# Optimization experiments

Hardware: AMD Instinct MI355X
Metric: run time of the kernel (lower is better)

Reference implementation:

```python
import jax, jax.numpy as jnp
import numpy as np

N = 100000      # nodes
E = 6400000     # edges (avg degree 64)
S = 8           # FSM states
X = 2 ** S      # neighborhood 'characters' (256)
ITERS = 20      # NeuralFSM.iterations


def setup_inputs() -> dict:
    key = jax.random.key(0)
    k1, k2, k3 = jax.random.split(key, 3)
    # one-hot initial node states [N, S]
    state_idx = jax.random.randint(k1, (N,), 0, S)
    s0 = jax.nn.one_hot(state_idx, S, dtype=jnp.float32)
    # edge list [2, E]
    edge_index = jax.random.randint(k2, (2, E), 0, N, dtype=jnp.int32)
    # FSM transition tensor T[char, state, :] is one-hot over next state -> [X, S, S]
    next_state = jax.random.randint(k3, (X, S), 0, S)
    T = jax.nn.one_hot(next_state, S, dtype=jnp.float32)
    return {"s0": s0, "edge_index": edge_index, "T": T}


def reference(s0, edge_index, T):
    n_nodes, n_states = s0.shape
    src, dst = edge_index[0], edge_index[1]
    powers = (2 ** jnp.arange(n_states)).astype(jnp.int32)  # base-2 encoding of thresholded aggr

    def step(s, _):
        # message = x_j gathered from source nodes, scatter-added at destinations
        msg_sum = jax.ops.segment_sum(s[src], dst, num_segments=n_nodes)  # [N, S]
        # threshold (> 0.5) then clamp to {0,1}
        aggr = (msg_sum > 0.5).astype(jnp.int32)                          # [N, S]
        # multiple-hot -> index into 2^S characters (one-hot folded into a gather)
        idx = aggr @ powers                                               # [N]
        # einsum('x,s,xst->t') with one-hot char == gather T[idx] then contract state
        new_s = jnp.einsum('ns,nst->nt', s, T[idx])                       # [N, S]
        return new_s, None

    s_final, _ = jax.lax.scan(step, s0, None, length=ITERS)
    return s_final
```

## Files before the change

### kernel.cpp

```cpp
#include <hip/hip_runtime.h>
#include <hip/hip_bf16.h>
#include <stdint.h>


#define NN 100000
#define EE 6400000
#define NCHARS 2048
#define ITERS 20

#define NBKT 250
#define NPB 400
#define WPS 12500
#define X4N 3125
#define CEDGE 12800
#define NCHUNK 500
#define PCAP 13312

#define BLINES 25
#define BAR_ARR(i) ((i) * 16)
#define BAR_TOP    800
#define BAR_REL(i) (832 + (i) * 16)
#define BAR_WORDS  2048

typedef uint32_t u32x4 __attribute__((ext_vector_type(4)));

__global__ void decode_kernel(const float* __restrict__ s0,
                              const float* __restrict__ T,
                              uint32_t* __restrict__ gPk0,
                              uint8_t* __restrict__ nextT,
                              uint32_t* __restrict__ bar) {
    int i = blockIdx.x * blockDim.x + threadIdx.x;
    int stride = gridDim.x * blockDim.x;
    for (int j = i; j < BAR_WORDS; j += stride) bar[j] = 0u;
    if (i < NCHARS) {
        const float* row = T + i * 8;
        int t = 0;
        #pragma unroll
        for (int k = 1; k < 8; ++k) if (row[k] > 0.5f) t = k;
        nextT[i] = (uint8_t)t;
    }
    for (int j = i; j < WPS; j += stride) {
        uint32_t wv = 0;
        const float* rows = s0 + (size_t)j * 64;
        #pragma unroll
        for (int k = 0; k < 8; ++k) {
            const float* row = rows + k * 8;
            int s = 0;
            #pragma unroll
            for (int q = 1; q < 8; ++q) if (row[q] > 0.5f) s = q;
            wv |= (uint32_t)s << (k << 2);
        }
        gPk0[j] = wv;
    }
}

__global__ void __launch_bounds__(512) p1_hist(const int* __restrict__ dst,
                                               uint32_t* __restrict__ hist) {
    __shared__ uint32_t cw[8][256];
    int t = threadIdx.x, w = t >> 6;
    int c = blockIdx.x;
    for (int i = t; i < 8 * 256; i += 512) ((uint32_t*)cw)[i] = 0;
    __syncthreads();
    const int4* p = (const int4*)(dst + c * CEDGE);
    for (int i = t; i < CEDGE / 4; i += 512) {
        int4 d = p[i];
        atomicAdd(&cw[w][d.x / NPB], 1u);
        atomicAdd(&cw[w][d.y / NPB], 1u);
        atomicAdd(&cw[w][d.z / NPB], 1u);
        atomicAdd(&cw[w][d.w / NPB], 1u);
    }
    __syncthreads();
    for (int b = t; b < NBKT; b += 512) {
        uint32_t s = 0;
        #pragma unroll
        for (int w2 = 0; w2 < 8; ++w2) s += cw[w2][b];
        hist[(size_t)c * NBKT + b] = s;
    }
}

__global__ void p2a_scan(uint32_t* __restrict__ hist, uint32_t* __restrict__ total) {
    __shared__ uint32_t lds[256];
    int t = threadIdx.x;
    int b = blockIdx.x;
    uint32_t carry = 0;
    for (int c0 = 0; c0 < NCHUNK; c0 += 256) {
        int c = c0 + t;
        uint32_t v = (c < NCHUNK) ? hist[(size_t)c * NBKT + b] : 0u;
        lds[t] = v;
        __syncthreads();
        for (int off = 1; off < 256; off <<= 1) {
            uint32_t x = (t >= off) ? lds[t - off] : 0u;
            __syncthreads();
            lds[t] += x;
            __syncthreads();
        }
        if (c < NCHUNK) hist[(size_t)c * NBKT + b] = lds[t] - v + carry;
        uint32_t tot = lds[255];
        __syncthreads();
        carry += tot;
    }
    if (t == 0) total[b] = carry;
}

__global__ void p2b_scan(const uint32_t* __restrict__ total,
                         uint32_t* __restrict__ bucket_base) {
    __shared__ uint32_t lds[512];
    int t = threadIdx.x;
    uint32_t v = (t < NBKT) ? total[t] : 0u;
    lds[t] = v;
    __syncthreads();
    for (int off = 1; off < 512; off <<= 1) {
        uint32_t x = (t >= off) ? lds[t - off] : 0u;
        __syncthreads();
        lds[t] += x;
        __syncthreads();
    }
    if (t < NBKT) bucket_base[t] = lds[t] - v;
    if (t == 511) bucket_base[NBKT] = lds[511];
}

__global__ void __launch_bounds__(512) p3_partition(const int* __restrict__ src,
                                                    const int* __restrict__ dst,
                                                    const uint32_t* __restrict__ hist,
                                                    const uint32_t* __restrict__ bucket_base,
                                                    uint32_t* __restrict__ csr) {
    __shared__ uint32_t stage[CEDGE];
    __shared__ uint32_t cw[8][256];
    __shared__ uint32_t loc[NBKT + 1];
    __shared__ uint32_t segoff[NBKT];
    __shared__ uint32_t scanb[512];
    int t = threadIdx.x, w = t >> 6;
    int c = blockIdx.x;
    int e0 = c * CEDGE;
    const int4* ps4 = (const int4*)(src + e0);
    const int4* pd4 = (const int4*)(dst + e0);
    for (int i = t; i < 8 * 256; i += 512) ((uint32_t*)cw)[i] = 0;
    __syncthreads();
    for (int i = t; i < CEDGE / 4; i += 512) {
        int4 d = pd4[i];
        atomicAdd(&cw[w][d.x / NPB], 1u);
        atomicAdd(&cw[w][d.y / NPB], 1u);
        atomicAdd(&cw[w][d.z / NPB], 1u);
        atomicAdd(&cw[w][d.w / NPB], 1u);
    }
    __syncthreads();
    uint32_t tot = 0;
    if (t < NBKT) {
        #pragma unroll
        for (int w2 = 0; w2 < 8; ++w2) tot += cw[w2][t];
    }
    scanb[t] = tot;
    __syncthreads();
    for (int off = 1; off < 512; off <<= 1) {
        uint32_t x = (t >= off) ? scanb[t - off] : 0u;
        __syncthreads();
        scanb[t] += x;
        __syncthreads();
    }
    if (t < NBKT) {
        uint32_t excl = scanb[t] - tot;
        loc[t] = excl;
        segoff[t] = bucket_base[t] + hist[(size_t)c * NBKT + t] - excl;
        uint32_t acc = excl;
        #pragma unroll
        for (int w2 = 0; w2 < 8; ++w2) {
            uint32_t cv = cw[w2][t];
            cw[w2][t] = acc;
            acc += cv;
        }
    }
    if (t == 0) loc[NBKT] = CEDGE;
    __syncthreads();
    for (int i = t; i < CEDGE / 4; i += 512) {
        int4 d = pd4[i];
        int4 s = ps4[i];
        int bb; uint32_t dl, pos;
        bb = d.x / NPB; dl = (uint32_t)(d.x - bb * NPB);
        pos = atomicAdd(&cw[w][bb], 1u); stage[pos] = ((uint32_t)s.x << 9) | dl;
        bb = d.y / NPB; dl = (uint32_t)(d.y - bb * NPB);
        pos = atomicAdd(&cw[w][bb], 1u); stage[pos] = ((uint32_t)s.y << 9) | dl;
        bb = d.z / NPB; dl = (uint32_t)(d.z - bb * NPB);
        pos = atomicAdd(&cw[w][bb], 1u); stage[pos] = ((uint32_t)s.z << 9) | dl;
        bb = d.w / NPB; dl = (uint32_t)(d.w - bb * NPB);
        pos = atomicAdd(&cw[w][bb], 1u); stage[pos] = ((uint32_t)s.w << 9) | dl;
    }
    __syncthreads();
    for (int i = t; i < CEDGE; i += 512) {
        int lo = 0, hi = NBKT;
        while (hi - lo > 1) { int mid = (lo + hi) >> 1; if (loc[mid] <= (uint32_t)i) lo = mid; else hi = mid; }
        csr[segoff[lo] + (uint32_t)i] = stage[i];
    }
}

__global__ void __launch_bounds__(512) p4_sortsrc(uint32_t* __restrict__ csr,
                                                  const uint32_t* __restrict__ bucket_base) {
    __shared__ uint32_t st[PCAP];
    __shared__ uint32_t binh[512];
    int t = threadIdx.x;
    int j = blockIdx.x;
    int b = j >> 1, h = j & 1;
    uint32_t base = bucket_base[b], endb = bucket_base[b + 1];
    uint32_t n = endb - base;
    uint32_t n1 = (n + 1) >> 1;
    uint32_t r0 = h ? base + n1 : base;
    uint32_t cnt = h ? n - n1 : n1;
    if (cnt > PCAP) return;
    for (uint32_t i = t; i < cnt; i += 512) st[i] = csr[r0 + i];
    binh[t] = 0;
    __syncthreads();
    for (uint32_t i = t; i < cnt; i += 512) atomicAdd(&binh[st[i] >> 17], 1u);
    __syncthreads();
    uint32_t v = binh[t];
    __syncthreads();
    for (int off = 1; off < 512; off <<= 1) {
        uint32_t x = (t >= off) ? binh[t - off] : 0u;
        __syncthreads();
        binh[t] += x;
        __syncthreads();
    }
    uint32_t excl = binh[t] - v;
    __syncthreads();
    binh[t] = excl;
    __syncthreads();
    for (uint32_t i = t; i < cnt; i += 512) {
        uint32_t w = st[i];
        uint32_t pos = atomicAdd(&binh[w >> 17], 1u);
        csr[r0 + pos] = w;
    }
}

__global__ void __launch_bounds__(1024) mega_kernel(const uint32_t* __restrict__ csr,
                                                    const uint32_t* __restrict__ bucket_base,
                                                    uint32_t* __restrict__ gPkA,
                                                    uint32_t* __restrict__ gPkB,
                                                    const uint8_t* __restrict__ nextT,
                                                    float* __restrict__ out,
                                                    uint32_t* __restrict__ bar) {
    __shared__ uint32_t sPk[WPS];
    __shared__ uint32_t mask[NPB];
    __shared__ uint32_t packOwn[NPB / 8];
    __shared__ uint8_t  nT[NCHARS];
    __shared__ uint8_t  sown[NPB];
    int t = threadIdx.x;
    int b = blockIdx.x;
    uint32_t base = bucket_base[b];
    uint32_t end  = bucket_base[b + 1];

    if (t < 512) ((uint32_t*)nT)[t] = ((const uint32_t*)nextT)[t];
    const int line = b % BLINES;

    for (int p = 0; p < ITERS; ++p) {
        const uint32_t* curG = (p & 1) ? gPkB : gPkA;
        uint32_t*       nxtG = (p & 1) ? gPkA : gPkB;
        {
            const u32x4* g4 = (const u32x4*)curG;
            int i0 = t, i1 = t + 1024, i2 = t + 2048;
            int i3 = t + 3072; if (i3 > X4N - 1) i3 = X4N - 1;
            const u32x4 *p0 = g4 + i0, *p1 = g4 + i1, *p2 = g4 + i2, *p3 = g4 + i3;
            u32x4 a0, a1, a2, a3;
            asm volatile(
                "global_load_dwordx4 %0, %4, off sc1\n\t"
                "global_load_dwordx4 %1, %5, off sc1\n\t"
                "global_load_dwordx4 %2, %6, off sc1\n\t"
                "global_load_dwordx4 %3, %7, off sc1\n\t"
                "s_waitcnt vmcnt(0)"
                : "=&v"(a0), "=&v"(a1), "=&v"(a2), "=&v"(a3)
                : "v"(p0), "v"(p1), "v"(p2), "v"(p3)
                : "memory");
            u32x4* s4 = (u32x4*)sPk;
            s4[i0] = a0; s4[i1] = a1; s4[i2] = a2; s4[i3] = a3;
        }
        if (t < NPB) mask[t] = 0;
        if (t < NPB / 8) packOwn[t] = 0;
        __syncthreads();

        uint32_t e = base + t;
        for (; e + 3072 < end; e += 4096) {
            uint32_t w0 = csr[e], w1 = csr[e + 1024], w2 = csr[e + 2048], w3 = csr[e + 3072];
            uint32_t s0_ = w0 >> 9, s1_ = w1 >> 9, s2_ = w2 >> 9, s3_ = w3 >> 9;
            uint32_t n0 = (sPk[s0_ >> 3] >> ((s0_ & 7) << 2)) & 7u;
            uint32_t n1 = (sPk[s1_ >> 3] >> ((s1_ & 7) << 2)) & 7u;
            uint32_t n2 = (sPk[s2_ >> 3] >> ((s2_ & 7) << 2)) & 7u;
            uint32_t n3 = (sPk[s3_ >> 3] >> ((s3_ & 7) << 2)) & 7u;
            atomicOr(&mask[w0 & 511u], 1u << n0);
            atomicOr(&mask[w1 & 511u], 1u << n1);
            atomicOr(&mask[w2 & 511u], 1u << n2);
            atomicOr(&mask[w3 & 511u], 1u << n3);
        }
        for (; e < end; e += 1024) {
            uint32_t w = csr[e];
            uint32_t s_ = w >> 9;
            uint32_t nb = (sPk[s_ >> 3] >> ((s_ & 7) << 2)) & 7u;
            atomicOr(&mask[w & 511u], 1u << nb);
        }
        __syncthreads();

        if (t < NPB) {
            int node = b * NPB + t;
            uint32_t sOwn = (sPk[node >> 3] >> ((node & 7) << 2)) & 7u;
            uint8_t ns = nT[(mask[t] << 3) + sOwn];
            sown[t] = ns;
            atomicOr(&packOwn[t >> 3], (uint32_t)ns << ((t & 7) << 2));
        }
        __syncthreads();
        if (p < ITERS - 1) {
            if (t < NPB / 8)
                __hip_atomic_store(&nxtG[(NPB / 8) * b + t], packOwn[t],
                                   __ATOMIC_RELAXED, __HIP_MEMORY_SCOPE_AGENT);
            __syncthreads();
            if (t == 0) {
                uint32_t epoch = (uint32_t)(p + 1);
                uint32_t old = atomicAdd(&bar[BAR_ARR(line)], 1u);
                if (old + 1u == 10u * epoch) {
                    uint32_t told = atomicAdd(&bar[BAR_TOP], 1u);
                    if (told + 1u == (uint32_t)BLINES * epoch) {
                        for (int r = 0; r < BLINES; ++r)
                            atomicExch(&bar[BAR_REL(r)], epoch);
                    }
                }
                while (__hip_atomic_load(&bar[BAR_REL(line)], __ATOMIC_RELAXED,
                                         __HIP_MEMORY_SCOPE_AGENT) < epoch)
                    __builtin_amdgcn_s_sleep(16);
            }
            __syncthreads();
        }
    }
    __syncthreads();
    for (int f = t; f < NPB * 8; f += 1024) {
        int node = f >> 3;
        out[(size_t)b * (NPB * 8) + f] = ((f & 7) == (int)sown[node]) ? 1.f : 0.f;
    }
}

__global__ void fb_decode(const float* __restrict__ s0, const float* __restrict__ T,
                          uint8_t* __restrict__ state, uint8_t* __restrict__ nextT,
                          uint32_t* __restrict__ mask) {
    int i = blockIdx.x * blockDim.x + threadIdx.x;
    if (i < NCHARS) {
        const float* row = T + i * 8;
        int t = 0;
        #pragma unroll
        for (int k = 1; k < 8; ++k) if (row[k] > 0.5f) t = k;
        nextT[i] = (uint8_t)t;
    }
    if (i < NN) {
        const float* row = s0 + i * 8;
        int s = 0;
        #pragma unroll
        for (int k = 1; k < 8; ++k) if (row[k] > 0.5f) s = k;
        state[i] = (uint8_t)s;
        mask[i] = 0u;
    }
}
__global__ void fb_edge(const int* __restrict__ src, const int* __restrict__ dst,
                        const uint8_t* __restrict__ state, uint32_t* __restrict__ mask) {
    int i = blockIdx.x * blockDim.x + threadIdx.x;
    int stride = gridDim.x * blockDim.x;
    for (int e = i; e < EE; e += stride) atomicOr(&mask[dst[e]], 1u << state[src[e]]);
}
__global__ void fb_update(uint8_t* __restrict__ state, uint32_t* __restrict__ mask,
                          const uint8_t* __restrict__ nextT) {
    int i = blockIdx.x * blockDim.x + threadIdx.x;
    if (i < NN) {
        uint32_t m = mask[i];
        state[i] = nextT[(m << 3) + state[i]];
        mask[i] = 0u;
    }
}
__global__ void fb_output(const uint8_t* __restrict__ state, float* __restrict__ out) {
    int i = blockIdx.x * blockDim.x + threadIdx.x;
    if (i < NN) {
        int s = state[i];
        float4 lo = make_float4(s == 0 ? 1.f : 0.f, s == 1 ? 1.f : 0.f,
                                s == 2 ? 1.f : 0.f, s == 3 ? 1.f : 0.f);
        float4 hi = make_float4(s == 4 ? 1.f : 0.f, s == 5 ? 1.f : 0.f,
                                s == 6 ? 1.f : 0.f, s == 7 ? 1.f : 0.f);
        float4* o = (float4*)(out + (size_t)i * 8);
        o[0] = lo;
        o[1] = hi;
    }
}

extern "C" void kernel_launch(void* const* d_in, const int* in_sizes, int n_in,
                              void* d_out, int out_size, void* d_ws, size_t ws_size,
                              hipStream_t stream) {
    const float* s0  = (const float*)d_in[0];
    const int*   ei  = (const int*)d_in[1];
    const float* T   = (const float*)d_in[2];
    float*       out = (float*)d_out;
    const int* src = ei;
    const int* dst = ei + EE;

    uint8_t* basep = (uint8_t*)d_ws;
    size_t off = 0;
    auto alloc = [&](size_t sz) -> void* {
        void* p = basep + off;
        off += (sz + 255) & ~(size_t)255;
        return p;
    };
    uint32_t* csr         = (uint32_t*)alloc(sizeof(uint32_t) * EE);
    uint32_t* hist        = (uint32_t*)alloc(sizeof(uint32_t) * (size_t)NCHUNK * NBKT);
    uint32_t* total       = (uint32_t*)alloc(sizeof(uint32_t) * NBKT);
    uint32_t* bucket_base = (uint32_t*)alloc(sizeof(uint32_t) * (NBKT + 1));
    uint8_t*  nextT       = (uint8_t*)alloc(NCHARS);
    uint32_t* gPkA        = (uint32_t*)alloc(sizeof(uint32_t) * WPS);
    uint32_t* gPkB        = (uint32_t*)alloc(sizeof(uint32_t) * WPS);
    uint32_t* bar         = (uint32_t*)alloc(sizeof(uint32_t) * BAR_WORDS);
    bool have_ws = (off <= ws_size);

    if (have_ws) {
        decode_kernel<<<51, 256, 0, stream>>>(s0, T, gPkA, nextT, bar);
        p1_hist<<<NCHUNK, 512, 0, stream>>>(dst, hist);
        p2a_scan<<<NBKT, 256, 0, stream>>>(hist, total);
        p2b_scan<<<1, 512, 0, stream>>>(total, bucket_base);
        p3_partition<<<NCHUNK, 512, 0, stream>>>(src, dst, hist, bucket_base, csr);
        p4_sortsrc<<<NBKT * 2, 512, 0, stream>>>(csr, bucket_base);
        mega_kernel<<<NBKT, 1024, 0, stream>>>(csr, bucket_base, gPkA, gPkB,
                                               nextT, out, bar);
    } else {
        uint32_t* mask = (uint32_t*)d_ws;
        uint8_t*  nT   = (uint8_t*)d_ws + 400128;
        uint8_t*  st   = (uint8_t*)d_ws + 402432;
        fb_decode<<<391, 256, 0, stream>>>(s0, T, st, nT, mask);
        for (int it = 0; it < ITERS; ++it) {
            fb_edge<<<2048, 256, 0, stream>>>(src, dst, st, mask);
            fb_update<<<391, 256, 0, stream>>>(st, mask, nT);
        }
        fb_output<<<391, 256, 0, stream>>>(st, out);
    }
}
```

Measured before the change: 284.9 us.

## Fuse CSR build phases into one grid-synchronized kernel and fold src sort into mega kernel

Replaces the separate histogram, two scan kernels and partition kernel with a single build kernel that accumulates global bucket counts atomically, uses software grid barriers to compute bucket bases in one block, and claims per-chunk output offsets with an atomic cursor. The per-bucket source sort moves into the start of the persistent mega kernel. The intent is to remove several kernel launches and a second full read of dst. In exchange it relies on all 500 build blocks being co-resident for the spin barrier, which risks deadlock if they are not. The atomic cursor also makes chunk placement order nondeterministic, though the later per-bucket sort hides this.

```diff
diff --git a/kernel.cpp b/kernel.cpp
--- a/kernel.cpp
+++ b/kernel.cpp
@@ -14,24 +14,53 @@
 #define X4N 3125
 #define CEDGE 12800
 #define NCHUNK 500
-#define PCAP 13312
-
-#define BLINES 25
-#define BAR_ARR(i) ((i) * 16)
-#define BAR_TOP    800
-#define BAR_REL(i) (832 + (i) * 16)
-#define BAR_WORDS  2048
+#define HCAP 13312
+
+#define BLD_ARR(i)  ((i) * 16)
+#define BLD_TOP     800
+#define BLD_REL(i)  (832 + (i) * 16)
+#define MEG_ARR(i)  (1664 + (i) * 16)
+#define MEG_TOP     2080
+#define MEG_REL(i)  (2112 + (i) * 16)
+#define CNT_OFF     3072
+#define CUR_OFF     3328
+#define BAR_WORDS   4096
 
 typedef uint32_t u32x4 __attribute__((ext_vector_type(4)));
+
+__device__ inline uint32_t load_dw_sc1(const uint32_t* p) {
+    uint32_t v;
+    asm volatile("global_load_dword %0, %1, off sc1\n\ts_waitcnt vmcnt(0)"
+                 : "=v"(v) : "v"(p) : "memory");
+    return v;
+}
+
+__device__ inline void grid_barrier(uint32_t* bar, int line, uint32_t epoch,
+                                    uint32_t perline, uint32_t nlines,
+                                    int arrBase, int topOff, int relBase) {
+    __syncthreads();
+    if (threadIdx.x == 0) {
+        uint32_t old = atomicAdd(&bar[arrBase + line * 16], 1u);
+        if (old + 1u == perline * epoch) {
+            uint32_t told = atomicAdd(&bar[topOff], 1u);
+            if (told + 1u == nlines * epoch) {
+                for (uint32_t r = 0; r < nlines; ++r)
+                    atomicExch(&bar[relBase + r * 16], epoch);
+            }
+        }
+        while (__hip_atomic_load(&bar[relBase + line * 16], __ATOMIC_RELAXED,
+                                 __HIP_MEMORY_SCOPE_AGENT) < epoch)
+            __builtin_amdgcn_s_sleep(16);
+    }
+    __syncthreads();
+}
 
 __global__ void decode_kernel(const float* __restrict__ s0,
                               const float* __restrict__ T,
                               uint32_t* __restrict__ gPk0,
-                              uint8_t* __restrict__ nextT,
-                              uint32_t* __restrict__ bar) {
+                              uint8_t* __restrict__ nextT) {
     int i = blockIdx.x * blockDim.x + threadIdx.x;
     int stride = gridDim.x * blockDim.x;
-    for (int j = i; j < BAR_WORDS; j += stride) bar[j] = 0u;
     if (i < NCHARS) {
         const float* row = T + i * 8;
         int t = 0;
@@ -54,86 +83,25 @@
     }
 }
 
-__global__ void __launch_bounds__(512) p1_hist(const int* __restrict__ dst,
-                                               uint32_t* __restrict__ hist) {
-    __shared__ uint32_t cw[8][256];
-    int t = threadIdx.x, w = t >> 6;
-    int c = blockIdx.x;
-    for (int i = t; i < 8 * 256; i += 512) ((uint32_t*)cw)[i] = 0;
-    __syncthreads();
-    const int4* p = (const int4*)(dst + c * CEDGE);
-    for (int i = t; i < CEDGE / 4; i += 512) {
-        int4 d = p[i];
-        atomicAdd(&cw[w][d.x / NPB], 1u);
-        atomicAdd(&cw[w][d.y / NPB], 1u);
-        atomicAdd(&cw[w][d.z / NPB], 1u);
-        atomicAdd(&cw[w][d.w / NPB], 1u);
-    }
-    __syncthreads();
-    for (int b = t; b < NBKT; b += 512) {
-        uint32_t s = 0;
-        #pragma unroll
-        for (int w2 = 0; w2 < 8; ++w2) s += cw[w2][b];
-        hist[(size_t)c * NBKT + b] = s;
-    }
-}
-
-__global__ void p2a_scan(uint32_t* __restrict__ hist, uint32_t* __restrict__ total) {
-    __shared__ uint32_t lds[256];
-    int t = threadIdx.x;
-    int b = blockIdx.x;
-    uint32_t carry = 0;
-    for (int c0 = 0; c0 < NCHUNK; c0 += 256) {
-        int c = c0 + t;
-        uint32_t v = (c < NCHUNK) ? hist[(size_t)c * NBKT + b] : 0u;
-        lds[t] = v;
-        __syncthreads();
-        for (int off = 1; off < 256; off <<= 1) {
-            uint32_t x = (t >= off) ? lds[t - off] : 0u;
-            __syncthreads();
-            lds[t] += x;
-            __syncthreads();
-        }
-        if (c < NCHUNK) hist[(size_t)c * NBKT + b] = lds[t] - v + carry;
-        uint32_t tot = lds[255];
-        __syncthreads();
-        carry += tot;
-    }
-    if (t == 0) total[b] = carry;
-}
-
-__global__ void p2b_scan(const uint32_t* __restrict__ total,
-                         uint32_t* __restrict__ bucket_base) {
-    __shared__ uint32_t lds[512];
-    int t = threadIdx.x;
-    uint32_t v = (t < NBKT) ? total[t] : 0u;
-    lds[t] = v;
-    __syncthreads();
-    for (int off = 1; off < 512; off <<= 1) {
-        uint32_t x = (t >= off) ? lds[t - off] : 0u;
-        __syncthreads();
-        lds[t] += x;
-        __syncthreads();
-    }
-    if (t < NBKT) bucket_base[t] = lds[t] - v;
-    if (t == 511) bucket_base[NBKT] = lds[511];
-}
-
-__global__ void __launch_bounds__(512) p3_partition(const int* __restrict__ src,
+__global__ void __launch_bounds__(512) build_kernel(const int* __restrict__ src,
                                                     const int* __restrict__ dst,
-                                                    const uint32_t* __restrict__ hist,
-                                                    const uint32_t* __restrict__ bucket_base,
-                                                    uint32_t* __restrict__ csr) {
+                                                    uint32_t* __restrict__ bucket_base,
+                                                    uint32_t* __restrict__ csr,
+                                                    uint32_t* __restrict__ bar) {
     __shared__ uint32_t stage[CEDGE];
     __shared__ uint32_t cw[8][256];
+    __shared__ uint32_t scanb[512];
     __shared__ uint32_t loc[NBKT + 1];
     __shared__ uint32_t segoff[NBKT];
-    __shared__ uint32_t scanb[512];
     int t = threadIdx.x, w = t >> 6;
     int c = blockIdx.x;
     int e0 = c * CEDGE;
     const int4* ps4 = (const int4*)(src + e0);
     const int4* pd4 = (const int4*)(dst + e0);
+    uint32_t* countsG = bar + CNT_OFF;
+    uint32_t* cursorG = bar + CUR_OFF;
+    const int line = c % 50;
+
     for (int i = t; i < 8 * 256; i += 512) ((uint32_t*)cw)[i] = 0;
     __syncthreads();
     for (int i = t; i < CEDGE / 4; i += 512) {
@@ -148,6 +116,7 @@
     if (t < NBKT) {
         #pragma unroll
         for (int w2 = 0; w2 < 8; ++w2) tot += cw[w2][t];
+        atomicAdd(&countsG[t], tot);
     }
     scanb[t] = tot;
     __syncthreads();
@@ -157,11 +126,37 @@
         scanb[t] += x;
         __syncthreads();
     }
+    if (t < NBKT) loc[t] = scanb[t] - tot;
+    if (t == 0) loc[NBKT] = CEDGE;
+
+    grid_barrier(bar, line, 1u, 10u, 50u, 0, BLD_TOP, 832);
+
+    if (c == 0) {
+        uint32_t v = 0;
+        if (t < NBKT) v = load_dw_sc1(&countsG[t]);
+        scanb[t] = v;
+        __syncthreads();
+        for (int off = 1; off < 512; off <<= 1) {
+            uint32_t x = (t >= off) ? scanb[t - off] : 0u;
+            __syncthreads();
+            scanb[t] += x;
+            __syncthreads();
+        }
+        if (t < NBKT)
+            __hip_atomic_store(&bucket_base[t], scanb[t] - v,
+                               __ATOMIC_RELAXED, __HIP_MEMORY_SCOPE_AGENT);
+        if (t == 0)
+            __hip_atomic_store(&bucket_base[NBKT], (uint32_t)EE,
+                               __ATOMIC_RELAXED, __HIP_MEMORY_SCOPE_AGENT);
+    }
+
+    grid_barrier(bar, line, 2u, 10u, 50u, 0, BLD_TOP, 832);
+
     if (t < NBKT) {
-        uint32_t excl = scanb[t] - tot;
-        loc[t] = excl;
-        segoff[t] = bucket_base[t] + hist[(size_t)c * NBKT + t] - excl;
-        uint32_t acc = excl;
+        uint32_t bb_ = load_dw_sc1(&bucket_base[t]);
+        uint32_t myStart = bb_ + atomicAdd(&cursorG[t], tot);
+        segoff[t] = myStart - loc[t];
+        uint32_t acc = loc[t];
         #pragma unroll
         for (int w2 = 0; w2 < 8; ++w2) {
             uint32_t cv = cw[w2][t];
@@ -169,7 +164,6 @@
             acc += cv;
         }
     }
-    if (t == 0) loc[NBKT] = CEDGE;
     __syncthreads();
     for (int i = t; i < CEDGE / 4; i += 512) {
         int4 d = pd4[i];
@@ -192,62 +186,63 @@
     }
 }
 
-__global__ void __launch_bounds__(512) p4_sortsrc(uint32_t* __restrict__ csr,
-                                                  const uint32_t* __restrict__ bucket_base) {
-    __shared__ uint32_t st[PCAP];
-    __shared__ uint32_t binh[512];
-    int t = threadIdx.x;
-    int j = blockIdx.x;
-    int b = j >> 1, h = j & 1;
-    uint32_t base = bucket_base[b], endb = bucket_base[b + 1];
-    uint32_t n = endb - base;
-    uint32_t n1 = (n + 1) >> 1;
-    uint32_t r0 = h ? base + n1 : base;
-    uint32_t cnt = h ? n - n1 : n1;
-    if (cnt > PCAP) return;
-    for (uint32_t i = t; i < cnt; i += 512) st[i] = csr[r0 + i];
-    binh[t] = 0;
-    __syncthreads();
-    for (uint32_t i = t; i < cnt; i += 512) atomicAdd(&binh[st[i] >> 17], 1u);
-    __syncthreads();
-    uint32_t v = binh[t];
-    __syncthreads();
-    for (int off = 1; off < 512; off <<= 1) {
-        uint32_t x = (t >= off) ? binh[t - off] : 0u;
-        __syncthreads();
-        binh[t] += x;
-        __syncthreads();
-    }
-    uint32_t excl = binh[t] - v;
-    __syncthreads();
-    binh[t] = excl;
-    __syncthreads();
-    for (uint32_t i = t; i < cnt; i += 512) {
-        uint32_t w = st[i];
-        uint32_t pos = atomicAdd(&binh[w >> 17], 1u);
-        csr[r0 + pos] = w;
-    }
-}
-
-__global__ void __launch_bounds__(1024) mega_kernel(const uint32_t* __restrict__ csr,
+__global__ void __launch_bounds__(1024) mega_kernel(uint32_t* __restrict__ csr,
                                                     const uint32_t* __restrict__ bucket_base,
                                                     uint32_t* __restrict__ gPkA,
                                                     uint32_t* __restrict__ gPkB,
                                                     const uint8_t* __restrict__ nextT,
                                                     float* __restrict__ out,
                                                     uint32_t* __restrict__ bar) {
-    __shared__ uint32_t sPk[WPS];
-    __shared__ uint32_t mask[NPB];
-    __shared__ uint32_t packOwn[NPB / 8];
-    __shared__ uint8_t  nT[NCHARS];
-    __shared__ uint8_t  sown[NPB];
+    __shared__ __align__(16) uint8_t shraw[55296];
+    __shared__ uint8_t nT[NCHARS];
+    __shared__ uint8_t sown[NPB];
     int t = threadIdx.x;
     int b = blockIdx.x;
     uint32_t base = bucket_base[b];
     uint32_t end  = bucket_base[b + 1];
 
     if (t < 512) ((uint32_t*)nT)[t] = ((const uint32_t*)nextT)[t];
-    const int line = b % BLINES;
+    const int line = b % 25;
+
+    {
+        uint32_t* st   = (uint32_t*)shraw;
+        uint32_t* binh = (uint32_t*)(shraw + 53248);
+        uint32_t n  = end - base;
+        uint32_t n1 = (n + 1) >> 1;
+        for (int h = 0; h < 2; ++h) {
+            uint32_t r0  = h ? base + n1 : base;
+            uint32_t cnt = h ? n - n1 : n1;
+            if (cnt <= (uint32_t)HCAP) {
+                for (uint32_t i = t; i < cnt; i += 1024) st[i] = csr[r0 + i];
+                if (t < 512) binh[t] = 0;
+                __syncthreads();
+                for (uint32_t i = t; i < cnt; i += 1024) atomicAdd(&binh[st[i] >> 17], 1u);
+                __syncthreads();
+                uint32_t v = (t < 512) ? binh[t] : 0u;
+                __syncthreads();
+                for (int off = 1; off < 512; off <<= 1) {
+                    uint32_t x = (t < 512 && t >= off) ? binh[t - off] : 0u;
+                    __syncthreads();
+                    if (t < 512) binh[t] += x;
+                    __syncthreads();
+                }
+                uint32_t excl = (t < 512) ? binh[t] - v : 0u;
+                __syncthreads();
+                if (t < 512) binh[t] = excl;
+                __syncthreads();
+                for (uint32_t i = t; i < cnt; i += 1024) {
+                    uint32_t wv = st[i];
+                    uint32_t pos = atomicAdd(&binh[wv >> 17], 1u);
+                    csr[r0 + pos] = wv;
+                }
+            }
+            __syncthreads();
+        }
+    }
+
+    uint32_t* sPk     = (uint32_t*)shraw;
+    uint32_t* mask    = (uint32_t*)(shraw + 50000);
+    uint32_t* packOwn = (uint32_t*)(shraw + 51600);
 
     for (int p = 0; p < ITERS; ++p) {
         const uint32_t* curG = (p & 1) ? gPkB : gPkA;
@@ -288,10 +283,10 @@
             atomicOr(&mask[w3 & 511u], 1u << n3);
         }
         for (; e < end; e += 1024) {
-            uint32_t w = csr[e];
-            uint32_t s_ = w >> 9;
+            uint32_t wv = csr[e];
+            uint32_t s_ = wv >> 9;
             uint32_t nb = (sPk[s_ >> 3] >> ((s_ & 7) << 2)) & 7u;
-            atomicOr(&mask[w & 511u], 1u << nb);
+            atomicOr(&mask[wv & 511u], 1u << nb);
         }
         __syncthreads();
 
@@ -307,22 +302,8 @@
             if (t < NPB / 8)
                 __hip_atomic_store(&nxtG[(NPB / 8) * b + t], packOwn[t],
                                    __ATOMIC_RELAXED, __HIP_MEMORY_SCOPE_AGENT);
-            __syncthreads();
-            if (t == 0) {
-                uint32_t epoch = (uint32_t)(p + 1);
-                uint32_t old = atomicAdd(&bar[BAR_ARR(line)], 1u);
-                if (old + 1u == 10u * epoch) {
-                    uint32_t told = atomicAdd(&bar[BAR_TOP], 1u);
-                    if (told + 1u == (uint32_t)BLINES * epoch) {
-                        for (int r = 0; r < BLINES; ++r)
-                            atomicExch(&bar[BAR_REL(r)], epoch);
-                    }
-                }
-                while (__hip_atomic_load(&bar[BAR_REL(line)], __ATOMIC_RELAXED,
-                                         __HIP_MEMORY_SCOPE_AGENT) < epoch)
-                    __builtin_amdgcn_s_sleep(16);
-            }
-            __syncthreads();
+            grid_barrier(bar, line, (uint32_t)(p + 1), 10u, 25u,
+                         1664, MEG_TOP, 2112);
         }
     }
     __syncthreads();
@@ -399,8 +380,6 @@
         return p;
     };
     uint32_t* csr         = (uint32_t*)alloc(sizeof(uint32_t) * EE);
-    uint32_t* hist        = (uint32_t*)alloc(sizeof(uint32_t) * (size_t)NCHUNK * NBKT);
-    uint32_t* total       = (uint32_t*)alloc(sizeof(uint32_t) * NBKT);
     uint32_t* bucket_base = (uint32_t*)alloc(sizeof(uint32_t) * (NBKT + 1));
     uint8_t*  nextT       = (uint8_t*)alloc(NCHARS);
     uint32_t* gPkA        = (uint32_t*)alloc(sizeof(uint32_t) * WPS);
@@ -409,12 +388,9 @@
     bool have_ws = (off <= ws_size);
 
     if (have_ws) {
-        decode_kernel<<<51, 256, 0, stream>>>(s0, T, gPkA, nextT, bar);
-        p1_hist<<<NCHUNK, 512, 0, stream>>>(dst, hist);
-        p2a_scan<<<NBKT, 256, 0, stream>>>(hist, total);
-        p2b_scan<<<1, 512, 0, stream>>>(total, bucket_base);
-        p3_partition<<<NCHUNK, 512, 0, stream>>>(src, dst, hist, bucket_base, csr);
-        p4_sortsrc<<<NBKT * 2, 512, 0, stream>>>(csr, bucket_base);
+        hipMemsetAsync(bar, 0, sizeof(uint32_t) * BAR_WORDS, stream);
+        decode_kernel<<<51, 256, 0, stream>>>(s0, T, gPkA, nextT);
+        build_kernel<<<NCHUNK, 512, 0, stream>>>(src, dst, bucket_base, csr, bar);
         mega_kernel<<<NBKT, 1024, 0, stream>>>(csr, bucket_base, gPkA, gPkB,
                                                nextT, out, bar);
     } else {
```

New measurement: 296.6 us. +4.1%, slower.

## Replace histogram+scan CSR build with fixed-capacity buckets and atomic cursors

Applied to the files above, without the earlier changes.

Removes the separate histogram pass and the two scan kernels. CSR buckets now get a fixed capacity per bucket and chunks claim their slots with global atomic cursors, so the destination array is read one time fewer and several launches go away. State and transition decoding is folded into the build kernel. The binary search for segment lookup is swapped for an LDS lookup table. The cost is padding per bucket and a non-deterministic edge order within a bucket. A bucket larger than its capacity would silently overflow, which is safe only for near-uniform degree distributions.

```diff
diff --git a/kernel.cpp b/kernel.cpp
--- a/kernel.cpp
+++ b/kernel.cpp
@@ -14,126 +14,74 @@
 #define X4N 3125
 #define CEDGE 12800
 #define NCHUNK 500
-#define PCAP 13312
-
-#define BLINES 25
-#define BAR_ARR(i) ((i) * 16)
-#define BAR_TOP    800
-#define BAR_REL(i) (832 + (i) * 16)
-#define BAR_WORDS  2048
+#define CAPB 27648
+#define HCAP 13824
+
+#define MEG_TOP     2080
+#define CUR_OFF     3328
+#define BAR_WORDS   4096
 
 typedef uint32_t u32x4 __attribute__((ext_vector_type(4)));
 
-__global__ void decode_kernel(const float* __restrict__ s0,
-                              const float* __restrict__ T,
-                              uint32_t* __restrict__ gPk0,
-                              uint8_t* __restrict__ nextT,
-                              uint32_t* __restrict__ bar) {
-    int i = blockIdx.x * blockDim.x + threadIdx.x;
-    int stride = gridDim.x * blockDim.x;
-    for (int j = i; j < BAR_WORDS; j += stride) bar[j] = 0u;
-    if (i < NCHARS) {
-        const float* row = T + i * 8;
-        int t = 0;
-        #pragma unroll
-        for (int k = 1; k < 8; ++k) if (row[k] > 0.5f) t = k;
-        nextT[i] = (uint8_t)t;
-    }
-    for (int j = i; j < WPS; j += stride) {
-        uint32_t wv = 0;
-        const float* rows = s0 + (size_t)j * 64;
-        #pragma unroll
-        for (int k = 0; k < 8; ++k) {
-            const float* row = rows + k * 8;
-            int s = 0;
-            #pragma unroll
-            for (int q = 1; q < 8; ++q) if (row[q] > 0.5f) s = q;
-            wv |= (uint32_t)s << (k << 2);
-        }
-        gPk0[j] = wv;
-    }
-}
-
-__global__ void __launch_bounds__(512) p1_hist(const int* __restrict__ dst,
-                                               uint32_t* __restrict__ hist) {
-    __shared__ uint32_t cw[8][256];
-    int t = threadIdx.x, w = t >> 6;
-    int c = blockIdx.x;
-    for (int i = t; i < 8 * 256; i += 512) ((uint32_t*)cw)[i] = 0;
-    __syncthreads();
-    const int4* p = (const int4*)(dst + c * CEDGE);
-    for (int i = t; i < CEDGE / 4; i += 512) {
-        int4 d = p[i];
-        atomicAdd(&cw[w][d.x / NPB], 1u);
-        atomicAdd(&cw[w][d.y / NPB], 1u);
-        atomicAdd(&cw[w][d.z / NPB], 1u);
-        atomicAdd(&cw[w][d.w / NPB], 1u);
-    }
-    __syncthreads();
-    for (int b = t; b < NBKT; b += 512) {
-        uint32_t s = 0;
-        #pragma unroll
-        for (int w2 = 0; w2 < 8; ++w2) s += cw[w2][b];
-        hist[(size_t)c * NBKT + b] = s;
-    }
-}
-
-__global__ void p2a_scan(uint32_t* __restrict__ hist, uint32_t* __restrict__ total) {
-    __shared__ uint32_t lds[256];
-    int t = threadIdx.x;
-    int b = blockIdx.x;
-    uint32_t carry = 0;
-    for (int c0 = 0; c0 < NCHUNK; c0 += 256) {
-        int c = c0 + t;
-        uint32_t v = (c < NCHUNK) ? hist[(size_t)c * NBKT + b] : 0u;
-        lds[t] = v;
-        __syncthreads();
-        for (int off = 1; off < 256; off <<= 1) {
-            uint32_t x = (t >= off) ? lds[t - off] : 0u;
-            __syncthreads();
-            lds[t] += x;
-            __syncthreads();
-        }
-        if (c < NCHUNK) hist[(size_t)c * NBKT + b] = lds[t] - v + carry;
-        uint32_t tot = lds[255];
-        __syncthreads();
-        carry += tot;
-    }
-    if (t == 0) total[b] = carry;
-}
-
-__global__ void p2b_scan(const uint32_t* __restrict__ total,
-                         uint32_t* __restrict__ bucket_base) {
-    __shared__ uint32_t lds[512];
-    int t = threadIdx.x;
-    uint32_t v = (t < NBKT) ? total[t] : 0u;
-    lds[t] = v;
-    __syncthreads();
-    for (int off = 1; off < 512; off <<= 1) {
-        uint32_t x = (t >= off) ? lds[t - off] : 0u;
-        __syncthreads();
-        lds[t] += x;
-        __syncthreads();
-    }
-    if (t < NBKT) bucket_base[t] = lds[t] - v;
-    if (t == 511) bucket_base[NBKT] = lds[511];
-}
-
-__global__ void __launch_bounds__(512) p3_partition(const int* __restrict__ src,
+__device__ inline void mega_barrier(uint32_t* bar, int line, uint32_t epoch) {
+    __syncthreads();
+    if (threadIdx.x == 0) {
+        uint32_t old = atomicAdd(&bar[1664 + line * 16], 1u);
+        if (old + 1u == 10u * epoch) {
+            uint32_t told = atomicAdd(&bar[MEG_TOP], 1u);
+            if (told + 1u == 25u * epoch) {
+                for (int r = 0; r < 25; ++r)
+                    atomicExch(&bar[2112 + r * 16], epoch);
+            }
+        }
+        while (__hip_atomic_load(&bar[2112 + line * 16], __ATOMIC_RELAXED,
+                                 __HIP_MEMORY_SCOPE_AGENT) < epoch)
+            __builtin_amdgcn_s_sleep(16);
+    }
+    __syncthreads();
+}
+
+__global__ void __launch_bounds__(512) build_kernel(const int* __restrict__ src,
                                                     const int* __restrict__ dst,
-                                                    const uint32_t* __restrict__ hist,
-                                                    const uint32_t* __restrict__ bucket_base,
-                                                    uint32_t* __restrict__ csr) {
+                                                    const float* __restrict__ s0,
+                                                    const float* __restrict__ T,
+                                                    uint32_t* __restrict__ gPk0,
+                                                    uint8_t* __restrict__ nextT,
+                                                    uint32_t* __restrict__ csr,
+                                                    uint32_t* __restrict__ bar) {
     __shared__ uint32_t stage[CEDGE];
     __shared__ uint32_t cw[8][256];
+    __shared__ uint32_t scanb[512];
     __shared__ uint32_t loc[NBKT + 1];
     __shared__ uint32_t segoff[NBKT];
-    __shared__ uint32_t scanb[512];
+    __shared__ uint8_t  lut[CEDGE];
     int t = threadIdx.x, w = t >> 6;
     int c = blockIdx.x;
     int e0 = c * CEDGE;
     const int4* ps4 = (const int4*)(src + e0);
     const int4* pd4 = (const int4*)(dst + e0);
+    uint32_t* cursorG = bar + CUR_OFF;
+
+    if (t < 25) loc[t] = 0;
+    __syncthreads();
+    if (t < 200) {
+        const float* row = s0 + ((size_t)c * 200 + t) * 8;
+        int s = 0;
+        #pragma unroll
+        for (int q = 1; q < 8; ++q) if (row[q] > 0.5f) s = q;
+        atomicOr(&loc[t >> 3], (uint32_t)s << ((t & 7) << 2));
+    }
+    __syncthreads();
+    if (t < 25) gPk0[c * 25 + t] = loc[t];
+    if (c < 4) {
+        const float* row = T + (c * 512 + t) * 8;
+        int s = 0;
+        #pragma unroll
+        for (int q = 1; q < 8; ++q) if (row[q] > 0.5f) s = q;
+        nextT[c * 512 + t] = (uint8_t)s;
+    }
+    __syncthreads();
+
     for (int i = t; i < 8 * 256; i += 512) ((uint32_t*)cw)[i] = 0;
     __syncthreads();
     for (int i = t; i < CEDGE / 4; i += 512) {
@@ -160,7 +108,8 @@
     if (t < NBKT) {
         uint32_t excl = scanb[t] - tot;
         loc[t] = excl;
-        segoff[t] = bucket_base[t] + hist[(size_t)c * NBKT + t] - excl;
+        uint32_t myStart = atomicAdd(&cursorG[t], tot);
+        segoff[t] = (uint32_t)t * CAPB + myStart - excl;
         uint32_t acc = excl;
         #pragma unroll
         for (int w2 = 0; w2 < 8; ++w2) {
@@ -171,6 +120,10 @@
     }
     if (t == 0) loc[NBKT] = CEDGE;
     __syncthreads();
+    for (int b = t; b < NBKT; b += 512) {
+        uint32_t lo = loc[b], hi = loc[b + 1];
+        for (uint32_t i = lo; i < hi; ++i) lut[i] = (uint8_t)b;
+    }
     for (int i = t; i < CEDGE / 4; i += 512) {
         int4 d = pd4[i];
         int4 s = ps4[i];
@@ -186,25 +139,22 @@
     }
     __syncthreads();
     for (int i = t; i < CEDGE; i += 512) {
-        int lo = 0, hi = NBKT;
-        while (hi - lo > 1) { int mid = (lo + hi) >> 1; if (loc[mid] <= (uint32_t)i) lo = mid; else hi = mid; }
-        csr[segoff[lo] + (uint32_t)i] = stage[i];
+        csr[segoff[lut[i]] + (uint32_t)i] = stage[i];
     }
 }
 
 __global__ void __launch_bounds__(512) p4_sortsrc(uint32_t* __restrict__ csr,
-                                                  const uint32_t* __restrict__ bucket_base) {
-    __shared__ uint32_t st[PCAP];
+                                                  const uint32_t* __restrict__ cntG) {
+    __shared__ uint32_t st[HCAP];
     __shared__ uint32_t binh[512];
     int t = threadIdx.x;
     int j = blockIdx.x;
     int b = j >> 1, h = j & 1;
-    uint32_t base = bucket_base[b], endb = bucket_base[b + 1];
-    uint32_t n = endb - base;
+    uint32_t n  = cntG[b];
     uint32_t n1 = (n + 1) >> 1;
-    uint32_t r0 = h ? base + n1 : base;
+    uint32_t r0 = (uint32_t)b * CAPB + (h ? n1 : 0);
     uint32_t cnt = h ? n - n1 : n1;
-    if (cnt > PCAP) return;
+    if (cnt > HCAP) return;
     for (uint32_t i = t; i < cnt; i += 512) st[i] = csr[r0 + i];
     binh[t] = 0;
     __syncthreads();
@@ -230,7 +180,6 @@
 }
 
 __global__ void __launch_bounds__(1024) mega_kernel(const uint32_t* __restrict__ csr,
-                                                    const uint32_t* __restrict__ bucket_base,
                                                     uint32_t* __restrict__ gPkA,
                                                     uint32_t* __restrict__ gPkB,
                                                     const uint8_t* __restrict__ nextT,
@@ -243,11 +192,11 @@
     __shared__ uint8_t  sown[NPB];
     int t = threadIdx.x;
     int b = blockIdx.x;
-    uint32_t base = bucket_base[b];
-    uint32_t end  = bucket_base[b + 1];
+    uint32_t base = (uint32_t)b * CAPB;
+    uint32_t end  = base + bar[CUR_OFF + b];
 
     if (t < 512) ((uint32_t*)nT)[t] = ((const uint32_t*)nextT)[t];
-    const int line = b % BLINES;
+    const int line = b % 25;
 
     for (int p = 0; p < ITERS; ++p) {
         const uint32_t* curG = (p & 1) ? gPkB : gPkA;
@@ -288,10 +237,10 @@
             atomicOr(&mask[w3 & 511u], 1u << n3);
         }
         for (; e < end; e += 1024) {
-            uint32_t w = csr[e];
-            uint32_t s_ = w >> 9;
+            uint32_t wv = csr[e];
+            uint32_t s_ = wv >> 9;
             uint32_t nb = (sPk[s_ >> 3] >> ((s_ & 7) << 2)) & 7u;
-            atomicOr(&mask[w & 511u], 1u << nb);
+            atomicOr(&mask[wv & 511u], 1u << nb);
         }
         __syncthreads();
 
@@ -307,22 +256,7 @@
             if (t < NPB / 8)
                 __hip_atomic_store(&nxtG[(NPB / 8) * b + t], packOwn[t],
                                    __ATOMIC_RELAXED, __HIP_MEMORY_SCOPE_AGENT);
-            __syncthreads();
-            if (t == 0) {
-                uint32_t epoch = (uint32_t)(p + 1);
-                uint32_t old = atomicAdd(&bar[BAR_ARR(line)], 1u);
-                if (old + 1u == 10u * epoch) {
-                    uint32_t told = atomicAdd(&bar[BAR_TOP], 1u);
-                    if (told + 1u == (uint32_t)BLINES * epoch) {
-                        for (int r = 0; r < BLINES; ++r)
-                            atomicExch(&bar[BAR_REL(r)], epoch);
-                    }
-                }
-                while (__hip_atomic_load(&bar[BAR_REL(line)], __ATOMIC_RELAXED,
-                                         __HIP_MEMORY_SCOPE_AGENT) < epoch)
-                    __builtin_amdgcn_s_sleep(16);
-            }
-            __syncthreads();
+            mega_barrier(bar, line, (uint32_t)(p + 1));
         }
     }
     __syncthreads();
@@ -398,25 +332,18 @@
         off += (sz + 255) & ~(size_t)255;
         return p;
     };
-    uint32_t* csr         = (uint32_t*)alloc(sizeof(uint32_t) * EE);
-    uint32_t* hist        = (uint32_t*)alloc(sizeof(uint32_t) * (size_t)NCHUNK * NBKT);
-    uint32_t* total       = (uint32_t*)alloc(sizeof(uint32_t) * NBKT);
-    uint32_t* bucket_base = (uint32_t*)alloc(sizeof(uint32_t) * (NBKT + 1));
-    uint8_t*  nextT       = (uint8_t*)alloc(NCHARS);
-    uint32_t* gPkA        = (uint32_t*)alloc(sizeof(uint32_t) * WPS);
-    uint32_t* gPkB        = (uint32_t*)alloc(sizeof(uint32_t) * WPS);
-    uint32_t* bar         = (uint32_t*)alloc(sizeof(uint32_t) * BAR_WORDS);
+    uint32_t* csr   = (uint32_t*)alloc(sizeof(uint32_t) * (size_t)NBKT * CAPB);
+    uint8_t*  nextT = (uint8_t*)alloc(NCHARS);
+    uint32_t* gPkA  = (uint32_t*)alloc(sizeof(uint32_t) * WPS);
+    uint32_t* gPkB  = (uint32_t*)alloc(sizeof(uint32_t) * WPS);
+    uint32_t* bar   = (uint32_t*)alloc(sizeof(uint32_t) * BAR_WORDS);
     bool have_ws = (off <= ws_size);
 
     if (have_ws) {
-        decode_kernel<<<51, 256, 0, stream>>>(s0, T, gPkA, nextT, bar);
-        p1_hist<<<NCHUNK, 512, 0, stream>>>(dst, hist);
-        p2a_scan<<<NBKT, 256, 0, stream>>>(hist, total);
-        p2b_scan<<<1, 512, 0, stream>>>(total, bucket_base);
-        p3_partition<<<NCHUNK, 512, 0, stream>>>(src, dst, hist, bucket_base, csr);
-        p4_sortsrc<<<NBKT * 2, 512, 0, stream>>>(csr, bucket_base);
-        mega_kernel<<<NBKT, 1024, 0, stream>>>(csr, bucket_base, gPkA, gPkB,
-                                               nextT, out, bar);
+        hipMemsetAsync(bar, 0, sizeof(uint32_t) * BAR_WORDS, stream);
+        build_kernel<<<NCHUNK, 512, 0, stream>>>(src, dst, s0, T, gPkA, nextT, csr, bar);
+        p4_sortsrc<<<NBKT * 2, 512, 0, stream>>>(csr, bar + CUR_OFF);
+        mega_kernel<<<NBKT, 1024, 0, stream>>>(csr, gPkA, gPkB, nextT, out, bar);
     } else {
         uint32_t* mask = (uint32_t*)d_ws;
         uint8_t*  nT   = (uint8_t*)d_ws + 400128;
```

Result: faster. 271.1 us (-4.9%).
